# Kernel optimization log

Hardware: AMD Instinct MI355X
Metric: run time of the kernel (lower is better)

Reference implementation:

```python
import jax, jax.numpy as jnp
import numpy as np

DIM = 384
HEADS = 12
HEAD_DIM = DIM // HEADS
SCALE = HEAD_DIM ** -0.5
HIDDEN = 4 * DIM
EPS = 1e-5


def _dwconv(x, w, b):
    # depthwise 3x3 conv, NCHW, kernel [C,1,3,3], groups=C
    y = jax.lax.conv_general_dilated(
        x, w, window_strides=(1, 1), padding='SAME',
        dimension_numbers=('NCHW', 'OIHW', 'NCHW'),
        feature_group_count=x.shape[1])
    return y + b[None, :, None, None]


def _layernorm(x, g, b):
    mu = jnp.mean(x, axis=-1, keepdims=True)
    var = jnp.mean(jnp.square(x - mu), axis=-1, keepdims=True)
    return (x - mu) * jax.lax.rsqrt(var + EPS) * g + b


def setup_inputs() -> dict:
    key = jax.random.key(0)
    ks = jax.random.split(key, 10)
    s = 0.02
    inp = {
        'x': jax.random.normal(ks[0], (32, DIM, 28, 28), dtype=jnp.float32),
        'cpe1_w': jax.random.normal(ks[1], (DIM, 1, 3, 3), dtype=jnp.float32) * s,
        'cpe1_b': jnp.zeros((DIM,), jnp.float32),
        'norm1_g': jnp.ones((DIM,), jnp.float32),
        'norm1_b': jnp.zeros((DIM,), jnp.float32),
        'qkv_w': jax.random.normal(ks[2], (3 * DIM, DIM), dtype=jnp.float32) * s,
        'proj_w': jax.random.normal(ks[3], (DIM, DIM), dtype=jnp.float32) * s,
        'proj_b': jnp.zeros((DIM,), jnp.float32),
        'cpe2_w': jax.random.normal(ks[4], (DIM, 1, 3, 3), dtype=jnp.float32) * s,
        'cpe2_b': jnp.zeros((DIM,), jnp.float32),
        'norm2_g': jnp.ones((DIM,), jnp.float32),
        'norm2_b': jnp.zeros((DIM,), jnp.float32),
        'fc1_w': jax.random.normal(ks[5], (HIDDEN, DIM), dtype=jnp.float32) * s,
        'fc1_b': jnp.zeros((HIDDEN,), jnp.float32),
        'fc2_w': jax.random.normal(ks[6], (DIM, HIDDEN), dtype=jnp.float32) * s,
        'fc2_b': jnp.zeros((DIM,), jnp.float32),
    }
    return inp


def reference(x, cpe1_w, cpe1_b, norm1_g, norm1_b, qkv_w, proj_w, proj_b,
              cpe2_w, cpe2_b, norm2_g, norm2_b, fc1_w, fc1_b, fc2_w, fc2_b):
    B, C, H, W = x.shape
    N = H * W
    # cpe1: depthwise conv residual (act = Identity)
    x = x + _dwconv(x, cpe1_w, cpe1_b)
    x = jnp.transpose(x.reshape(B, C, N), (0, 2, 1))  # [B, N, C]

    # channel attention
    cur = _layernorm(x, norm1_g, norm1_b)
    qkv = cur @ qkv_w.T  # [B, N, 3C]
    qkv = qkv.reshape(B, N, 3, HEADS, HEAD_DIM)
    q = qkv[:, :, 0]  # [B, N, h, d]
    k = qkv[:, :, 1] * SCALE
    v = qkv[:, :, 2]
    # attn = k^T @ v over tokens: [B, h, d, d]
    attn = jnp.einsum('bnhd,bnhe->bhde', k, v)
    attn = jax.nn.softmax(attn, axis=-1)
    # out[n,d] = sum_e attn[d,e] * q[n,e]
    out = jnp.einsum('bhde,bnhe->bnhd', attn, q).reshape(B, N, C)
    cur = out @ proj_w.T + proj_b
    x = x + cur

    # cpe2
    x = jnp.transpose(x, (0, 2, 1)).reshape(B, C, H, W)
    x = x + _dwconv(x, cpe2_w, cpe2_b)

    # MLP
    x = jnp.transpose(x.reshape(B, C, N), (0, 2, 1))  # [B, N, C]
    y = _layernorm(x, norm2_g, norm2_b)
    y = jax.nn.gelu(y @ fc1_w.T + fc1_b, approximate=False)
    y = y @ fc2_w.T + fc2_b
    x = x + y
    return jnp.transpose(x, (0, 2, 1)).reshape(B, C, H, W)
```

## Files before the change

kernel.cpp:

```cpp
#include <hip/hip_runtime.h>
#include <hip/hip_bf16.h>

#define CDIM 384
#define NHEADS 12
#define HDIM 32
#define HIDDEN 1536
#define BBATCH 32
#define HH 28
#define WW 28
#define NTOK 784
#define BN (BBATCH * NTOK)
#define LN_EPS 1e-5f
#define ATT_SCALE 0.17677669529663687f
#define YTILES 196
#define PERXCD 25

typedef __hip_bfloat16 bf16;
typedef __attribute__((ext_vector_type(8))) short bf16x8;
typedef __attribute__((ext_vector_type(4))) float f32x4;

__device__ __forceinline__ void stf(float* p, float v) { *p = v; }
__device__ __forceinline__ void stf(bf16* p, float v) { *p = __float2bfloat16(v); }

__device__ __forceinline__ short f2bs(float v) {
    bf16 t = __float2bfloat16(v);
    return *reinterpret_cast<short*>(&t);
}

__device__ __forceinline__ float bf2f(unsigned short u) {
    return __uint_as_float(((unsigned)u) << 16);
}

__device__ __forceinline__ float gelu_f(float x) {
    float u = x * (0.7978845608f + 0.0356774081f * x * x);
    float e = __expf(-2.f * u);
    return x / (1.f + e);
}

__device__ __forceinline__ void gload16(const void* g, void* l) {
    __builtin_amdgcn_global_load_lds(
        (const __attribute__((address_space(1))) unsigned int*)g,
        (__attribute__((address_space(3))) unsigned int*)l, 16, 0, 0);
}

__global__ __launch_bounds__(256) void prep_k(
    const float* __restrict__ w0, const float* __restrict__ w1,
    const float* __restrict__ w2, const float* __restrict__ w3,
    bf16* __restrict__ dst, const float* __restrict__ cw,
    float* __restrict__ cwt)
{
    int blk = blockIdx.x;
    if (blk >= 6912) {
        int i = (blk - 6912) * 256 + threadIdx.x;
        if (i < 9 * CDIM) {
            int k = i / CDIM, c = i % CDIM;
            cwt[i] = cw[c * 9 + k];
        }
        return;
    }
    int i = blk * 256 + threadIdx.x;
    const float* src; int off;
    if (i < 442368)       { src = w0; off = i; }
    else if (i < 589824)  { src = w1; off = i - 442368; }
    else if (i < 1179648) { src = w2; off = i - 589824; }
    else                  { src = w3; off = i - 1179648; }
    dst[i] = __float2bfloat16(src[off]);
}

__global__ __launch_bounds__(256) void cpe1_tr_v2(
    const float* __restrict__ x, const float* __restrict__ w,
    const float* __restrict__ bias, float* __restrict__ xt)
{
    __shared__ float sm[64][128];
    __shared__ float t2[64][69];
    int b = blockIdx.z;
    int n0 = blockIdx.y * 64;
    int c0 = blockIdx.x * 64;
    int tid = threadIdx.x;
    int nf0 = (n0 - 32) >> 2;

    const float4* xb = (const float4*)(x + ((size_t)b * CDIM + c0) * NTOK);
#pragma unroll
    for (int i = 0; i < 8; i++) {
        int q = tid + i * 256;
        int row = q >> 5, c4 = q & 31;
        int nf = nf0 + c4;
        float4 v = {0.f, 0.f, 0.f, 0.f};
        if ((unsigned)nf < (NTOK / 4)) v = xb[row * (NTOK / 4) + nf];
        *(float4*)&sm[row][c4 * 4] = v;
    }
    __syncthreads();

    int n_loc = tid & 63;
    int n = n0 + n_loc;
    int l = 32 + n_loc;
    if (n < NTOK) {
        int h = n / WW, wc = n % WW;
        bool hm = h > 0, hp = h < HH - 1, wm = wc > 0, wpv = wc < WW - 1;
        int cbase = tid >> 6;
#pragma unroll
        for (int j = 0; j < 16; j++) {
            int c_loc = cbase + j * 4;
            const float* wp = w + (c0 + c_loc) * 9;
            const float* s = sm[c_loc];
            float a = wp[4] * s[l];
            if (hm)        a += wp[1] * s[l - WW];
            if (hp)        a += wp[7] * s[l + WW];
            if (wm)        a += wp[3] * s[l - 1];
            if (wpv)       a += wp[5] * s[l + 1];
            if (hm && wm)  a += wp[0] * s[l - WW - 1];
            if (hm && wpv) a += wp[2] * s[l - WW + 1];
            if (hp && wm)  a += wp[6] * s[l + WW - 1];
            if (hp && wpv) a += wp[8] * s[l + WW + 1];
            t2[n_loc][c_loc] = s[l] + a + bias[c0 + c_loc];
        }
    }
    __syncthreads();

#pragma unroll
    for (int i = 0; i < 4; i++) {
        int q = tid + i * 256;
        int nl = q >> 4, c4 = q & 15;
        int nn = n0 + nl;
        if (nn < NTOK) {
            float4 v = *(const float4*)&t2[nl][c4 * 4];
            *(float4*)(xt + ((size_t)b * NTOK + nn) * CDIM + c0 + c4 * 4) = v;
        }
    }
}

__global__ __launch_bounds__(256) void ln1_k(
    const float* __restrict__ in, const float* __restrict__ g,
    const float* __restrict__ b, bf16* __restrict__ out)
{
    int tid = threadIdx.x;
    int l = tid & 31;
    size_t tok = (size_t)blockIdx.x * 8 + (tid >> 5);
    const float4* row = (const float4*)(in + tok * CDIM);
    float4 v[3];
    float s = 0.f;
#pragma unroll
    for (int j = 0; j < 3; j++) {
        v[j] = row[l + j * 32];
        s += v[j].x + v[j].y + v[j].z + v[j].w;
    }
#pragma unroll
    for (int off = 16; off >= 1; off >>= 1) s += __shfl_xor(s, off);
    float mu = s * (1.f / CDIM);
    float q = 0.f;
#pragma unroll
    for (int j = 0; j < 3; j++) {
        float dx = v[j].x - mu, dy = v[j].y - mu;
        float dz = v[j].z - mu, dw = v[j].w - mu;
        q += dx * dx + dy * dy + dz * dz + dw * dw;
    }
#pragma unroll
    for (int off = 16; off >= 1; off >>= 1) q += __shfl_xor(q, off);
    float rs = rsqrtf(q * (1.f / CDIM) + LN_EPS);
    const float4* g4 = (const float4*)g;
    const float4* b4 = (const float4*)b;
    ushort4* o4 = (ushort4*)(out + tok * CDIM);
#pragma unroll
    for (int j = 0; j < 3; j++) {
        int idx = l + j * 32;
        float4 gv = g4[idx], bv = b4[idx];
        ushort4 r;
        r.x = (unsigned short)f2bs((v[j].x - mu) * rs * gv.x + bv.x);
        r.y = (unsigned short)f2bs((v[j].y - mu) * rs * gv.y + bv.y);
        r.z = (unsigned short)f2bs((v[j].z - mu) * rs * gv.z + bv.z);
        r.w = (unsigned short)f2bs((v[j].w - mu) * rs * gv.w + bv.w);
        o4[idx] = r;
    }
}

__global__ __launch_bounds__(256) void cpe2_ln_fused(
    const float* __restrict__ xin, const float* __restrict__ wt,
    const float* __restrict__ cbias, const float* __restrict__ g,
    const float* __restrict__ b, float* __restrict__ x3,
    bf16* __restrict__ lnout)
{
    __shared__ float wts[9 * CDIM];
    int tid = threadIdx.x;
    for (int i = tid; i < 864; i += 256)
        ((float4*)wts)[i] = ((const float4*)wt)[i];
    __syncthreads();
    int l = tid & 31;
    size_t tok = (size_t)blockIdx.x * 8 + (tid >> 5);
    int n = (int)(tok % NTOK);
    int h = n / WW, wc = n % WW;
    bool hm = h > 0, hp = h < HH - 1, wm = wc > 0, wpv = wc < WW - 1;
    const float* row = xin + tok * CDIM;
    const float4* w4 = (const float4*)wts;
    float4 ctr[3], acc[3];
#pragma unroll
    for (int j = 0; j < 3; j++) {
        int idx = l + j * 32;
        ctr[j] = ((const float4*)row)[idx];
        float4 ww = w4[4 * 96 + idx];
        acc[j].x = ww.x * ctr[j].x; acc[j].y = ww.y * ctr[j].y;
        acc[j].z = ww.z * ctr[j].z; acc[j].w = ww.w * ctr[j].w;
    }
#define TAP(k, cond, dn)                                                     \
    if (cond) {                                                              \
        const float4* rp = (const float4*)(row + (dn) * CDIM);               \
        _Pragma("unroll")                                                    \
        for (int j = 0; j < 3; j++) {                                        \
            int idx = l + j * 32;                                            \
            float4 vv = rp[idx];                                             \
            float4 ww = w4[(k) * 96 + idx];                                  \
            acc[j].x = fmaf(ww.x, vv.x, acc[j].x);                           \
            acc[j].y = fmaf(ww.y, vv.y, acc[j].y);                           \
            acc[j].z = fmaf(ww.z, vv.z, acc[j].z);                           \
            acc[j].w = fmaf(ww.w, vv.w, acc[j].w);                           \
        }                                                                    \
    }
    TAP(0, hm && wm,   -WW - 1)
    TAP(1, hm,         -WW)
    TAP(2, hm && wpv,  -WW + 1)
    TAP(3, wm,         -1)
    TAP(5, wpv,        1)
    TAP(6, hp && wm,   WW - 1)
    TAP(7, hp,         WW)
    TAP(8, hp && wpv,  WW + 1)
#undef TAP
    float s = 0.f;
    float4 val[3];
    float4* x3r = (float4*)(x3 + tok * CDIM);
#pragma unroll
    for (int j = 0; j < 3; j++) {
        int idx = l + j * 32;
        float4 cb = ((const float4*)cbias)[idx];
        val[j].x = ctr[j].x + acc[j].x + cb.x;
        val[j].y = ctr[j].y + acc[j].y + cb.y;
        val[j].z = ctr[j].z + acc[j].z + cb.z;
        val[j].w = ctr[j].w + acc[j].w + cb.w;
        x3r[idx] = val[j];
        s += val[j].x + val[j].y + val[j].z + val[j].w;
    }
#pragma unroll
    for (int off = 16; off >= 1; off >>= 1) s += __shfl_xor(s, off);
    float mu = s * (1.f / CDIM);
    float q = 0.f;
#pragma unroll
    for (int j = 0; j < 3; j++) {
        float dx = val[j].x - mu, dy = val[j].y - mu;
        float dz = val[j].z - mu, dw = val[j].w - mu;
        q += dx * dx + dy * dy + dz * dz + dw * dw;
    }
#pragma unroll
    for (int off = 16; off >= 1; off >>= 1) q += __shfl_xor(q, off);
    float rs = rsqrtf(q * (1.f / CDIM) + LN_EPS);
    const float4* g4 = (const float4*)g;
    const float4* b4 = (const float4*)b;
    ushort4* o4 = (ushort4*)(lnout + tok * CDIM);
#pragma unroll
    for (int j = 0; j < 3; j++) {
        int idx = l + j * 32;
        float4 gv = g4[idx], bv = b4[idx];
        ushort4 r;
        r.x = (unsigned short)f2bs((val[j].x - mu) * rs * gv.x + bv.x);
        r.y = (unsigned short)f2bs((val[j].y - mu) * rs * gv.y + bv.y);
        r.z = (unsigned short)f2bs((val[j].z - mu) * rs * gv.z + bv.z);
        r.w = (unsigned short)f2bs((val[j].w - mu) * rs * gv.w + bv.w);
        o4[idx] = r;
    }
}

template <int ACT, bool RES, typename TO, bool OUTT, int K>
__global__ __launch_bounds__(256, 4) void gemm_mfma(
    const short* __restrict__ Abf, const short* __restrict__ Bw,
    const float* __restrict__ bias, const float* __restrict__ res,
    TO* __restrict__ Co, int M, int NX)
{
    int id = blockIdx.x;
    int xcd = id & 7, slot_ = id >> 3;
    int yloc = slot_ / NX, xx = slot_ - yloc * NX;
    int y = xcd * PERXCD + yloc;
    if (y >= YTILES) return;

    __shared__ __align__(16) short lds[16896];
    const int tid = threadIdx.x;
    const int wid = tid >> 6, lane = tid & 63;
    const int wrow = wid >> 1, wcol = wid & 1;
    const int quad = lane >> 4, lr = lane & 15;
    const int r0 = y * 128, m0 = xx * 128;

    const int srow = lane >> 2;
    const int sg   = (lane & 3) ^ ((lane >> 3) & 3);
    const short* gA = Abf + (size_t)(r0 + wid * 32 + srow) * K + sg * 8;
    const short* gB = Bw  + (size_t)(m0 + wid * 32 + srow) * K + sg * 8;

    auto stage = [&](int k0, int p) {
        short* lA = lds + p * 8192 + wid * 1024;
        short* lB = lds + p * 8192 + 4096 + wid * 1024;
#pragma unroll
        for (int k = 0; k < 2; k++) {
            gload16(gA + k0 + (size_t)k * 16 * K, lA + k * 512);
            gload16(gB + k0 + (size_t)k * 16 * K, lB + k * 512);
        }
    };

    const int slot = (quad ^ ((lr >> 1) & 3)) * 8;
    int fA[4], fB[4];
#pragma unroll
    for (int i = 0; i < 4; i++) {
        fA[i] = (wrow * 64 + i * 16 + lr) * 32 + slot;
        fB[i] = 4096 + (wcol * 64 + i * 16 + lr) * 32 + slot;
    }

    f32x4 acc[4][4] = {};

    stage(0, 0);
    int p = 0;
    for (int k0 = 0; k0 < K; k0 += 32) {
        __syncthreads();
        if (k0 + 32 < K) stage(k0 + 32, p ^ 1);
        const short* As = lds + p * 8192;
        bf16x8 av[4], bv[4];
#pragma unroll
        for (int i = 0; i < 4; i++) {
            av[i] = *(const bf16x8*)(As + fA[i]);
            bv[i] = *(const bf16x8*)(As + fB[i]);
        }
#pragma unroll
        for (int i = 0; i < 4; i++)
#pragma unroll
            for (int j = 0; j < 4; j++)
                acc[i][j] = __builtin_amdgcn_mfma_f32_16x16x32_bf16(
                    av[i], bv[j], acc[i][j], 0, 0, 0);
        p ^= 1;
    }

    if constexpr (OUTT) {
        float* Csf = (float*)lds;
        __syncthreads();
#pragma unroll
        for (int pass = 0; pass < 2; pass++) {
            if (wcol == pass) {
#pragma unroll
                for (int i = 0; i < 4; i++) {
                    int lrow = wrow * 64 + i * 16 + quad * 4;
#pragma unroll
                    for (int j = 0; j < 4; j++) {
                        int lcol = j * 16 + lr;
                        int gc = m0 + pass * 64 + lcol;
                        float bb = bias ? bias[gc] : 0.f;
#pragma unroll
                        for (int rr = 0; rr < 4; rr++) {
                            float v = acc[i][j][rr] + bb;
                            if (RES)
                                v += res[(size_t)(r0 + lrow + rr) * M + gc];
                            if (ACT == 1) v = gelu_f(v);
                            Csf[(lrow + rr) * 66 + lcol] = v;
                        }
                    }
                }
            }
            __syncthreads();
            int tok = tid & 127;
            int csel = tid >> 7;
            int gtok = r0 + tok;
            int bb2 = gtok / NTOK;
            int nn2 = gtok - bb2 * NTOK;
#pragma unroll
            for (int s = 0; s < 32; s++) {
                int cl = s * 2 + csel;
                int gcol = m0 + pass * 64 + cl;
                Co[((size_t)bb2 * CDIM + gcol) * NTOK + nn2] = Csf[tok * 66 + cl];
            }
            __syncthreads();
        }
    } else if constexpr (sizeof(TO) == 4) {
#pragma unroll
        for (int i = 0; i < 4; i++) {
            int gr = r0 + wrow * 64 + i * 16 + quad * 4;
#pragma unroll
            for (int j = 0; j < 4; j++) {
                int gc = m0 + wcol * 64 + j * 16 + lr;
                float bb = bias ? bias[gc] : 0.f;
#pragma unroll
                for (int rr = 0; rr < 4; rr++) {
                    size_t idx = (size_t)(gr + rr) * M + gc;
                    float v = acc[i][j][rr] + bb;
                    if (RES) v += res[idx];
                    if (ACT == 1) v = gelu_f(v);
                    stf((float*)&Co[idx], v);
                }
            }
        }
    } else {
        __syncthreads();
        short* Cs = lds;
#pragma unroll
        for (int i = 0; i < 4; i++) {
            int lrow = wrow * 64 + i * 16 + quad * 4;
#pragma unroll
            for (int j = 0; j < 4; j++) {
                int lcol = wcol * 64 + j * 16 + lr;
                float bb = bias ? bias[m0 + lcol] : 0.f;
#pragma unroll
                for (int rr = 0; rr < 4; rr++) {
                    float v = acc[i][j][rr] + bb;
                    if (ACT == 1) v = gelu_f(v);
                    Cs[(lrow + rr) * 132 + lcol] = f2bs(v);
                }
            }
        }
        __syncthreads();
        short* co = (short*)Co;
#pragma unroll
        for (int s = 0; s < 16; s++) {
            int row = s * 8 + (tid >> 5);
            int seg = tid & 31;
            uint2 vv = *(const uint2*)(Cs + row * 132 + seg * 4);
            *(uint2*)(co + (size_t)(r0 + row) * M + m0 + seg * 4) = vv;
        }
    }
}

__global__ __launch_bounds__(256) void attn_k(
    const bf16* __restrict__ qkv, float* __restrict__ attn)
{
    int bh = blockIdx.x;
    int b = bh / NHEADS, h = bh % NHEADS;
    __shared__ float ks[64][32];
    __shared__ float vs[64][32];
    __shared__ float sm[32][33];
    int tid = threadIdx.x;
    int d = tid >> 3, e0 = (tid & 7) * 4;
    int nn = tid >> 2, q8 = (tid & 3) * 8;
    float acc[4] = {0.f, 0.f, 0.f, 0.f};
    for (int n0 = 0; n0 < NTOK; n0 += 64) {
        int n = n0 + nn;
        float kv[8], vv[8];
        if (n < NTOK) {
            const unsigned short* base =
                (const unsigned short*)qkv + ((size_t)b * NTOK + n) * (3 * CDIM);
            uint4 kq = *(const uint4*)(base + CDIM + h * HDIM + q8);
            uint4 vq = *(const uint4*)(base + 2 * CDIM + h * HDIM + q8);
            const unsigned short* kp = (const unsigned short*)&kq;
            const unsigned short* vp = (const unsigned short*)&vq;
#pragma unroll
            for (int j = 0; j < 8; j++) {
                kv[j] = ATT_SCALE * bf2f(kp[j]);
                vv[j] = bf2f(vp[j]);
            }
        } else {
#pragma unroll
            for (int j = 0; j < 8; j++) { kv[j] = 0.f; vv[j] = 0.f; }
        }
        *(float4*)&ks[nn][q8]     = make_float4(kv[0], kv[1], kv[2], kv[3]);
        *(float4*)&ks[nn][q8 + 4] = make_float4(kv[4], kv[5], kv[6], kv[7]);
        *(float4*)&vs[nn][q8]     = make_float4(vv[0], vv[1], vv[2], vv[3]);
        *(float4*)&vs[nn][q8 + 4] = make_float4(vv[4], vv[5], vv[6], vv[7]);
        __syncthreads();
#pragma unroll 8
        for (int k = 0; k < 64; k++) {
            float kd = ks[k][d];
            float4 vv4 = *(const float4*)&vs[k][e0];
            acc[0] = fmaf(kd, vv4.x, acc[0]);
            acc[1] = fmaf(kd, vv4.y, acc[1]);
            acc[2] = fmaf(kd, vv4.z, acc[2]);
            acc[3] = fmaf(kd, vv4.w, acc[3]);
        }
        __syncthreads();
    }
#pragma unroll
    for (int j = 0; j < 4; j++) sm[d][e0 + j] = acc[j];
    __syncthreads();
    if (tid < 32) {
        float mx = -1e30f;
#pragma unroll
        for (int e = 0; e < 32; e++) mx = fmaxf(mx, sm[tid][e]);
        float ssum = 0.f;
        float ex[32];
#pragma unroll
        for (int e = 0; e < 32; e++) { ex[e] = expf(sm[tid][e] - mx); ssum += ex[e]; }
        float inv = 1.f / ssum;
        float* arow = attn + ((size_t)bh * 32 + tid) * 32;
#pragma unroll
        for (int e = 0; e < 32; e++) arow[e] = ex[e] * inv;
    }
}

__global__ __launch_bounds__(384) void apply_attn_k(
    const bf16* __restrict__ qkv, const float* __restrict__ attn,
    bf16* __restrict__ out)
{
    int b = blockIdx.x;
    int chunk = blockIdx.y;
    int tid = threadIdx.x;
    int h = tid >> 5;
    __shared__ float qs[8][CDIM];
    float at[32];
    const float4* ap = (const float4*)(attn + ((size_t)(b * NHEADS) * 32 + tid) * 32);
#pragma unroll
    for (int e4 = 0; e4 < 8; e4++) {
        float4 v = ap[e4];
        at[e4 * 4 + 0] = v.x; at[e4 * 4 + 1] = v.y;
        at[e4 * 4 + 2] = v.z; at[e4 * 4 + 3] = v.w;
    }
    int row8 = tid / 48;
    int seg = tid - row8 * 48;
    int nbase = chunk * 56;
    for (int t0 = 0; t0 < 56; t0 += 8) {
        __syncthreads();
        {
            int n = nbase + t0 + row8;
            const unsigned short* src =
                (const unsigned short*)qkv + ((size_t)b * NTOK + n) * (3 * CDIM) + seg * 8;
            uint4 qv = *(const uint4*)src;
            const unsigned short* qp = (const unsigned short*)&qv;
            *(float4*)&qs[row8][seg * 8] =
                make_float4(bf2f(qp[0]), bf2f(qp[1]), bf2f(qp[2]), bf2f(qp[3]));
            *(float4*)&qs[row8][seg * 8 + 4] =
                make_float4(bf2f(qp[4]), bf2f(qp[5]), bf2f(qp[6]), bf2f(qp[7]));
        }
        __syncthreads();
#pragma unroll
        for (int i = 0; i < 8; i++) {
            const float4* q4 = (const float4*)&qs[i][h * 32];
            float s = 0.f;
#pragma unroll
            for (int e4 = 0; e4 < 8; e4++) {
                float4 qv = q4[e4];
                s = fmaf(at[e4 * 4 + 0], qv.x, s);
                s = fmaf(at[e4 * 4 + 1], qv.y, s);
                s = fmaf(at[e4 * 4 + 2], qv.z, s);
                s = fmaf(at[e4 * 4 + 3], qv.w, s);
            }
            int n = nbase + t0 + i;
            out[((size_t)b * NTOK + n) * CDIM + tid] = __float2bfloat16(s);
        }
    }
}

extern "C" void kernel_launch(void* const* d_in, const int* in_sizes, int n_in,
                              void* d_out, int out_size, void* d_ws, size_t ws_size,
                              hipStream_t stream) {
    const float* x      = (const float*)d_in[0];
    const float* cpe1_w = (const float*)d_in[1];
    const float* cpe1_b = (const float*)d_in[2];
    const float* n1g    = (const float*)d_in[3];
    const float* n1b    = (const float*)d_in[4];
    const float* qkv_w  = (const float*)d_in[5];
    const float* proj_w = (const float*)d_in[6];
    const float* proj_b = (const float*)d_in[7];
    const float* cpe2_w = (const float*)d_in[8];
    const float* cpe2_b = (const float*)d_in[9];
    const float* n2g    = (const float*)d_in[10];
    const float* n2b    = (const float*)d_in[11];
    const float* fc1_w  = (const float*)d_in[12];
    const float* fc1_b  = (const float*)d_in[13];
    const float* fc2_w  = (const float*)d_in[14];
    const float* fc2_b  = (const float*)d_in[15];

    const size_t A = (size_t)BN * CDIM;
    const size_t HA = A / 2;

    bf16* wqkv  = (bf16*)d_ws;
    bf16* wproj = wqkv + 442368;
    bf16* wfc1  = wproj + 147456;
    bf16* wfc2  = wfc1 + 589824;
    float* base = (float*)d_ws + 884736;

    float* xt        = base;
    bf16*  curb      = (bf16*)(base + A);
    bf16*  ylnb      = (bf16*)(base + A);
    bf16*  qkvb      = (bf16*)(base + A + HA);
    float* x3        = base + A + HA;
    bf16*  h1        = (bf16*)(base + A + HA + A);
    float* attnm     = base + 3 * A;
    bf16*  attn_outb = (bf16*)(base + 3 * A + 393216);
    float* cpe2_wt   = base + (A * 9) / 2;

    const int GEMM_GRID3  = 8 * PERXCD * 3;
    const int GEMM_GRID9  = 8 * PERXCD * 9;
    const int GEMM_GRID12 = 8 * PERXCD * 12;

    prep_k<<<6926, 256, 0, stream>>>(qkv_w, proj_w, fc1_w, fc2_w, wqkv,
                                     cpe2_w, cpe2_wt);

    cpe1_tr_v2<<<dim3(CDIM / 64, 13, BBATCH), 256, 0, stream>>>(
        x, cpe1_w, cpe1_b, xt);
    ln1_k<<<BN / 8, 256, 0, stream>>>(xt, n1g, n1b, curb);
    gemm_mfma<0, false, bf16, false, 384><<<GEMM_GRID9, 256, 0, stream>>>(
        (const short*)curb, (const short*)wqkv, nullptr, nullptr, qkvb, 1152, 9);
    attn_k<<<BBATCH * NHEADS, 256, 0, stream>>>(qkvb, attnm);
    apply_attn_k<<<dim3(BBATCH, 14), 384, 0, stream>>>(qkvb, attnm, attn_outb);
    gemm_mfma<0, true, float, false, 384><<<GEMM_GRID3, 256, 0, stream>>>(
        (const short*)attn_outb, (const short*)wproj, proj_b, xt, xt, 384, 3);
    cpe2_ln_fused<<<BN / 8, 256, 0, stream>>>(xt, cpe2_wt, cpe2_b, n2g, n2b,
                                              x3, ylnb);
    gemm_mfma<1, false, bf16, false, 384><<<GEMM_GRID12, 256, 0, stream>>>(
        (const short*)ylnb, (const short*)wfc1, fc1_b, nullptr, h1, 1536, 12);
    gemm_mfma<0, true, float, true, 1536><<<GEMM_GRID3, 256, 0, stream>>>(
        (const short*)h1, (const short*)wfc2, fc2_b, x3, (float*)d_out, 384, 3);
}
```

Baseline: 436.2 us.

## Restructure cpe1 conv-transpose kernel with 32-channel tiles and direct stores

Halves the channel tile of the first depthwise-conv plus transpose kernel to 32, doubling the block count. Weights and bias are staged in shared memory and then held in registers per thread. The second shared-memory transpose buffer and its barrier are removed, so each thread writes its output directly. The output stores are now 32 consecutive floats (128 bytes) per token row instead of float4 rows of 64 channels, which may coalesce less well. The shared tile is also padded to avoid bank conflicts.

```diff
diff --git a/kernel.cpp b/kernel.cpp
--- a/kernel.cpp
+++ b/kernel.cpp
@@ -67,64 +67,61 @@
     dst[i] = __float2bfloat16(src[off]);
 }
 
-__global__ __launch_bounds__(256) void cpe1_tr_v2(
+__global__ __launch_bounds__(256) void cpe1_tr_v3(
     const float* __restrict__ x, const float* __restrict__ w,
     const float* __restrict__ bias, float* __restrict__ xt)
 {
-    __shared__ float sm[64][128];
-    __shared__ float t2[64][69];
+    __shared__ float sm[32][130];
+    __shared__ float wls[32][10];
+    __shared__ float bls[32];
     int b = blockIdx.z;
     int n0 = blockIdx.y * 64;
-    int c0 = blockIdx.x * 64;
+    int c0 = blockIdx.x * 32;
     int tid = threadIdx.x;
     int nf0 = (n0 - 32) >> 2;
 
+    for (int i = tid; i < 288; i += 256) wls[i / 9][i % 9] = w[c0 * 9 + i];
+    if (tid < 32) bls[tid] = bias[c0 + tid];
+
     const float4* xb = (const float4*)(x + ((size_t)b * CDIM + c0) * NTOK);
 #pragma unroll
-    for (int i = 0; i < 8; i++) {
+    for (int i = 0; i < 4; i++) {
         int q = tid + i * 256;
         int row = q >> 5, c4 = q & 31;
         int nf = nf0 + c4;
         float4 v = {0.f, 0.f, 0.f, 0.f};
-        if ((unsigned)nf < (NTOK / 4)) v = xb[row * (NTOK / 4) + nf];
-        *(float4*)&sm[row][c4 * 4] = v;
+        if ((unsigned)nf < (NTOK >> 2)) v = xb[(size_t)row * (NTOK >> 2) + nf];
+        float2* p = (float2*)&sm[row][c4 * 4];
+        p[0] = make_float2(v.x, v.y);
+        p[1] = make_float2(v.z, v.w);
     }
     __syncthreads();
 
-    int n_loc = tid & 63;
-    int n = n0 + n_loc;
-    int l = 32 + n_loc;
-    if (n < NTOK) {
-        int h = n / WW, wc = n % WW;
-        bool hm = h > 0, hp = h < HH - 1, wm = wc > 0, wpv = wc < WW - 1;
-        int cbase = tid >> 6;
-#pragma unroll
-        for (int j = 0; j < 16; j++) {
-            int c_loc = cbase + j * 4;
-            const float* wp = w + (c0 + c_loc) * 9;
-            const float* s = sm[c_loc];
-            float a = wp[4] * s[l];
-            if (hm)        a += wp[1] * s[l - WW];
-            if (hp)        a += wp[7] * s[l + WW];
-            if (wm)        a += wp[3] * s[l - 1];
-            if (wpv)       a += wp[5] * s[l + 1];
-            if (hm && wm)  a += wp[0] * s[l - WW - 1];
-            if (hm && wpv) a += wp[2] * s[l - WW + 1];
-            if (hp && wm)  a += wp[6] * s[l + WW - 1];
-            if (hp && wpv) a += wp[8] * s[l + WW + 1];
-            t2[n_loc][c_loc] = s[l] + a + bias[c0 + c_loc];
-        }
-    }
-    __syncthreads();
-
-#pragma unroll
-    for (int i = 0; i < 4; i++) {
-        int q = tid + i * 256;
-        int nl = q >> 4, c4 = q & 15;
-        int nn = n0 + nl;
-        if (nn < NTOK) {
-            float4 v = *(const float4*)&t2[nl][c4 * 4];
-            *(float4*)(xt + ((size_t)b * NTOK + nn) * CDIM + c0 + c4 * 4) = v;
+    int c = tid & 31;
+    int tsub = tid >> 5;
+    float wr[9];
+#pragma unroll
+    for (int k = 0; k < 9; k++) wr[k] = wls[c][k];
+    float bb = bls[c];
+    const float* s = sm[c];
+#pragma unroll
+    for (int it = 0; it < 8; it++) {
+        int tok = it * 8 + tsub;
+        int n = n0 + tok;
+        if (n < NTOK) {
+            int h = n / WW, wc = n % WW;
+            bool hm = h > 0, hp = h < HH - 1, wm = wc > 0, wpv = wc < WW - 1;
+            int l = 32 + tok;
+            float a = wr[4] * s[l];
+            if (hm)        a += wr[1] * s[l - WW];
+            if (hp)        a += wr[7] * s[l + WW];
+            if (wm)        a += wr[3] * s[l - 1];
+            if (wpv)       a += wr[5] * s[l + 1];
+            if (hm && wm)  a += wr[0] * s[l - WW - 1];
+            if (hm && wpv) a += wr[2] * s[l - WW + 1];
+            if (hp && wm)  a += wr[6] * s[l + WW - 1];
+            if (hp && wpv) a += wr[8] * s[l + WW + 1];
+            xt[((size_t)b * NTOK + n) * CDIM + c0 + c] = s[l] + a + bb;
         }
     }
 }
@@ -581,7 +578,7 @@
     prep_k<<<6926, 256, 0, stream>>>(qkv_w, proj_w, fc1_w, fc2_w, wqkv,
                                      cpe2_w, cpe2_wt);
 
-    cpe1_tr_v2<<<dim3(CDIM / 64, 13, BBATCH), 256, 0, stream>>>(
+    cpe1_tr_v3<<<dim3(CDIM / 32, 13, BBATCH), 256, 0, stream>>>(
         x, cpe1_w, cpe1_b, xt);
     ln1_k<<<BN / 8, 256, 0, stream>>>(xt, n1g, n1b, curb);
     gemm_mfma<0, false, bf16, false, 384><<<GEMM_GRID9, 256, 0, stream>>>(
```

Result: faster. 402.6 us (-7.7%).
